# Performance work log

Hardware: AMD Instinct MI355X
Metric: run time of the kernel (lower is better)

## Reference

```python
import jax, jax.numpy as jnp
import numpy as np

# Static problem dims (match setup_inputs / torch max()+1 derivation)
N = 2_000_000      # atoms
NALT = 8           # alternatives
B, C, R = 8, 4, 512  # batch, chains, residues
N_ATOM_TYPES = 500
VDW_COL = 0        # property_hashings['solvenergy_props']['VdW']
PADDING_INDEX = -1
BACKBONE_ATOMS = (0, 1, 2, 3)


def setup_inputs() -> dict:
    key = jax.random.key(0)
    k1, k2, k3, k4, k5, k6, k7, k8 = jax.random.split(key, 8)
    at_name = jax.random.randint(k1, (N,), 0, 40)      # atom type hashes (first 4 = backbone)
    batch = jax.random.randint(k2, (N,), 0, B)
    chain = jax.random.randint(k3, (N,), 0, C)
    resnum = jax.random.randint(k4, (N,), 0, R)
    atom_description = jnp.stack([at_name, batch, chain, resnum], axis=1).astype(jnp.int64)
    return {
        "coords": jax.random.normal(k5, (N, 3), dtype=jnp.float32),
        "atom_description": atom_description,
        "alternativeMask": jax.random.randint(k6, (N, NALT), 0, 2).astype(bool),
        "facc": jax.random.uniform(k7, (N, NALT), dtype=jnp.float32),
        "atom_Properties": jax.random.uniform(k8, (N_ATOM_TYPES, 8), dtype=jnp.float32),
        "weight": jnp.zeros((1,), dtype=jnp.float32),
    }


def reference(coords, atom_description, alternativeMask, facc, atom_Properties, weight):
    at_name = atom_description[:, 0]
    b_idx = atom_description[:, 1]
    c_idx = atom_description[:, 2]
    r_idx = atom_description[:, 3]

    # is_backbone: OR over backbone atom hashes
    bb = jnp.asarray(BACKBONE_ATOMS)
    is_backbone = (at_name[:, None] == bb[None, :]).any(axis=-1)  # [N]

    # bindToAtoms: gather VdW property, masked multiply by max(facc, 0)
    sa = jnp.maximum(facc, jnp.float32(0.0))                 # [N, NALT]
    vdw = atom_Properties[at_name, VDW_COL]                  # [N]
    atomE = jnp.where(alternativeMask, vdw[:, None] * sa, jnp.float32(0.0))
    atomE = atomE * (1.0 - jnp.tanh(weight[0])) * 0.3        # [N, NALT]

    # bindToResi: masked scatter-add into [B, C, R, NALT]
    valid = r_idx != PADDING_INDEX
    mc_vals = jnp.where((is_backbone & valid)[:, None], atomE, jnp.float32(0.0))
    sc_vals = jnp.where((~is_backbone & valid)[:, None], atomE, jnp.float32(0.0))
    zeros = jnp.zeros((B, C, R, NALT), dtype=jnp.float32)
    finalMC = zeros.at[b_idx, c_idx, r_idx].add(mc_vals)
    finalSC = zeros.at[b_idx, c_idx, r_idx].add(sc_vals)
    return finalMC, finalSC
```

## Files before the change

kernel.cpp:

```cpp
#include <hip/hip_runtime.h>
#include <hip/hip_bf16.h>
#include <math.h>

#define NALT      8
#define BDIM      8
#define CDIM      4
#define RDIM      512
#define OUT_HALF  (BDIM * CDIM * RDIM * NALT)
#define OUT_TOTAL (2 * OUT_HALF)

#define NBUCKET   32
#define BLK_ATOMS 512
#define AITER     2
#define NWAVE     4
#define LSLOTS    8192


__device__ __forceinline__ unsigned int pack_bf16_2(float a, float b) {
    unsigned int ua = __float_as_uint(a);
    unsigned int ub = __float_as_uint(b);
    ua = (ua + 0x7fffu + ((ua >> 16) & 1u)) >> 16;
    ub = (ub + 0x7fffu + ((ub >> 16) & 1u)) >> 16;
    return ua | (ub << 16);
}

__global__ void __launch_bounds__(256) vdw_fused_kernel(
    const int4*   __restrict__ desc,
    const int4*   __restrict__ mask,
    const float4* __restrict__ facc,
    const float*  __restrict__ props,
    const float*  __restrict__ weight,
    unsigned short* __restrict__ hdrArr,
    unsigned short* __restrict__ lidxArr,
    uint4*        __restrict__ valArr,
    int n)
{
    __shared__ unsigned int   cw[NWAVE][NBUCKET];
    __shared__ unsigned int   base[NBUCKET + 1];
    __shared__ unsigned short s_lidx[BLK_ATOMS];
    __shared__ uint4          s_val[BLK_ATOMS];

    const int tid  = threadIdx.x;
    const int w    = tid >> 6;
    const int lane = tid & 63;
    if (lane < NBUCKET) cw[w][lane] = 0;

    const int a0 = blockIdx.x * BLK_ATOMS;
    int4   d_[AITER];
    float4 f0_[AITER], f1_[AITER];
    int4   m0_[AITER], m1_[AITER];
    bool   ok[AITER];
    #pragma unroll
    for (int it = 0; it < AITER; ++it) {
        const int a  = a0 + it * 256 + tid;
        ok[it] = (a < n);
        const int aa = ok[it] ? a : (n - 1);
        d_[it]  = desc[aa];
        f0_[it] = facc[aa * 2 + 0];
        f1_[it] = facc[aa * 2 + 1];
        m0_[it] = mask[aa * 2 + 0];
        m1_[it] = mask[aa * 2 + 1];
    }
    const float scale = (1.0f - tanhf(weight[0])) * 0.3f;

    int bkt[AITER];
    int lidx[AITER];
    #pragma unroll
    for (int it = 0; it < AITER; ++it) {
        const int4 d = d_[it];
        bkt[it] = -1;
        if (ok[it] && d.w != -1) {
            bkt[it]  = d.y * CDIM + d.z;
            lidx[it] = ((d.x < 4) ? 0 : 4096) + d.w * 8;
            atomicAdd(&cw[w][bkt[it]], 1u);
        }
    }

    uint4 rv[AITER];
    #pragma unroll
    for (int it = 0; it < AITER; ++it) {
        if (bkt[it] < 0) continue;
        const float vs = props[d_[it].x * 8] * scale;
        const float4 f0 = f0_[it], f1 = f1_[it];
        const int4   m0 = m0_[it], m1 = m1_[it];
        const float v0 = m0.x ? vs * fmaxf(f0.x, 0.0f) : 0.0f;
        const float v1 = m0.y ? vs * fmaxf(f0.y, 0.0f) : 0.0f;
        const float v2 = m0.z ? vs * fmaxf(f0.z, 0.0f) : 0.0f;
        const float v3 = m0.w ? vs * fmaxf(f0.w, 0.0f) : 0.0f;
        const float v4 = m1.x ? vs * fmaxf(f1.x, 0.0f) : 0.0f;
        const float v5 = m1.y ? vs * fmaxf(f1.y, 0.0f) : 0.0f;
        const float v6 = m1.z ? vs * fmaxf(f1.z, 0.0f) : 0.0f;
        const float v7 = m1.w ? vs * fmaxf(f1.w, 0.0f) : 0.0f;
        rv[it] = make_uint4(pack_bf16_2(v0, v1), pack_bf16_2(v2, v3),
                            pack_bf16_2(v4, v5), pack_bf16_2(v6, v7));
    }
    __syncthreads();

    if (tid < NBUCKET) {
        unsigned int s = 0;
        #pragma unroll
        for (int ww = 0; ww < NWAVE; ++ww) {
            const unsigned int c = cw[ww][tid];
            cw[ww][tid] = s;
            s += c;
        }
        unsigned int incl = s;
        #pragma unroll
        for (int off = 1; off < NBUCKET; off <<= 1) {
            const unsigned int t = __shfl_up(incl, off, NBUCKET);
            if (tid >= off) incl += t;
        }
        base[tid] = incl - s;
        if (tid == NBUCKET - 1) base[NBUCKET] = incl;
    }
    __syncthreads();

    #pragma unroll
    for (int it = 0; it < AITER; ++it) {
        if (bkt[it] < 0) continue;
        const unsigned int pos = base[bkt[it]] + atomicAdd(&cw[w][bkt[it]], 1u);
        s_lidx[pos] = (unsigned short)lidx[it];
        s_val[pos]  = rv[it];
    }
    __syncthreads();

    if (tid <= NBUCKET)
        hdrArr[blockIdx.x * 64 + tid] = (unsigned short)base[tid];

    unsigned int* ldst = (unsigned int*)(lidxArr + (size_t)blockIdx.x * BLK_ATOMS);
    const unsigned int* lsrc = (const unsigned int*)s_lidx;
    #pragma unroll
    for (int k = 0; k < BLK_ATOMS / 2 / 256; ++k)
        ldst[k * 256 + tid] = lsrc[k * 256 + tid];

    uint4* vdst = valArr + (size_t)blockIdx.x * BLK_ATOMS;
    #pragma unroll
    for (int k = 0; k < BLK_ATOMS / 256; ++k)
        vdst[k * 256 + tid] = s_val[k * 256 + tid];
}

__global__ void __launch_bounds__(256) vdw_accum_kernel(
    const unsigned short* __restrict__ hdrArr,
    const unsigned short* __restrict__ lidxArr,
    const uint4*          __restrict__ valArr,
    float*                __restrict__ partial,
    int nblocks, int nsplit)
{
    __shared__ float acc[LSLOTS];
    const int tid = threadIdx.x;
    for (int k = tid; k < LSLOTS; k += 256) acc[k] = 0.0f;
    __syncthreads();

    const int bucket = blockIdx.x / nsplit;
    const int split  = blockIdx.x % nsplit;
    const int per = (nblocks + nsplit - 1) / nsplit;
    const int b0  = split * per;
    const int b1  = (b0 + per < nblocks) ? (b0 + per) : nblocks;

    const int g    = tid >> 5;
    const int lane = tid & 31;

    for (int blk = b0 + g; blk < b1; blk += 8) {
        const int start = hdrArr[blk * 64 + bucket];
        const int end   = hdrArr[blk * 64 + bucket + 1];
        const unsigned short* la = lidxArr + (size_t)blk * BLK_ATOMS;
        const uint4*          va = valArr  + (size_t)blk * BLK_ATOMS;
        for (int rec = start + lane; rec < end; rec += 32) {
            const int   l = la[rec];
            const uint4 v = va[rec];
            float t;
            t = __uint_as_float(v.x << 16);          if (t != 0.0f) atomicAdd(&acc[l + 0], t);
            t = __uint_as_float(v.x & 0xffff0000u);  if (t != 0.0f) atomicAdd(&acc[l + 1], t);
            t = __uint_as_float(v.y << 16);          if (t != 0.0f) atomicAdd(&acc[l + 2], t);
            t = __uint_as_float(v.y & 0xffff0000u);  if (t != 0.0f) atomicAdd(&acc[l + 3], t);
            t = __uint_as_float(v.z << 16);          if (t != 0.0f) atomicAdd(&acc[l + 4], t);
            t = __uint_as_float(v.z & 0xffff0000u);  if (t != 0.0f) atomicAdd(&acc[l + 5], t);
            t = __uint_as_float(v.w << 16);          if (t != 0.0f) atomicAdd(&acc[l + 6], t);
            t = __uint_as_float(v.w & 0xffff0000u);  if (t != 0.0f) atomicAdd(&acc[l + 7], t);
        }
    }
    __syncthreads();

    float* dst = partial + (size_t)blockIdx.x * LSLOTS;
    for (int k = tid; k < LSLOTS; k += 256) dst[k] = acc[k];
}

__global__ void __launch_bounds__(256) vdw_merge_kernel(
    const float* __restrict__ partial,
    float*       __restrict__ out,
    int nsplit)
{
    const int idx = blockIdx.x * 256 + threadIdx.x;
    if (idx >= OUT_TOTAL) return;
    const int bb     = idx >> 17;
    const int b      = (idx >> 14) & 7;
    const int c      = (idx >> 12) & 3;
    const int lidx   = bb * 4096 + (idx & 4095);
    const int bucket = b * CDIM + c;
    const float* p = partial + ((size_t)bucket * nsplit) * LSLOTS + lidx;
    float s = 0.0f;
    for (int sp = 0; sp < nsplit; ++sp)
        s += p[(size_t)sp * LSLOTS];
    out[idx] = s;
}

__global__ void __launch_bounds__(256) vdw_atomic_kernel(
    const int*   __restrict__ desc,
    const int*   __restrict__ mask,
    const float* __restrict__ facc,
    const float* __restrict__ props,
    const float* __restrict__ weight,
    float*       __restrict__ out,
    int n)
{
    const int i = blockIdx.x * blockDim.x + threadIdx.x;
    if (i >= n) return;
    const float scale = (1.0f - tanhf(weight[0])) * 0.3f;
    const int4 d = reinterpret_cast<const int4*>(desc)[i];
    if (d.w == -1) return;
    const float vs = props[d.x * 8 + 0] * scale;
    const int   bb = (d.x >= 0 && d.x <= 3) ? 0 : 1;
    float* base = out + bb * OUT_HALF + (((d.y * CDIM + d.z) * RDIM + d.w) * NALT);
    const float4 f0 = reinterpret_cast<const float4*>(facc)[i * 2 + 0];
    const float4 f1 = reinterpret_cast<const float4*>(facc)[i * 2 + 1];
    const int4   m0 = reinterpret_cast<const int4*>(mask)[i * 2 + 0];
    const int4   m1 = reinterpret_cast<const int4*>(mask)[i * 2 + 1];
    if (m0.x) atomicAdd(base + 0, vs * fmaxf(f0.x, 0.0f));
    if (m0.y) atomicAdd(base + 1, vs * fmaxf(f0.y, 0.0f));
    if (m0.z) atomicAdd(base + 2, vs * fmaxf(f0.z, 0.0f));
    if (m0.w) atomicAdd(base + 3, vs * fmaxf(f0.w, 0.0f));
    if (m1.x) atomicAdd(base + 4, vs * fmaxf(f1.x, 0.0f));
    if (m1.y) atomicAdd(base + 5, vs * fmaxf(f1.y, 0.0f));
    if (m1.z) atomicAdd(base + 6, vs * fmaxf(f1.z, 0.0f));
    if (m1.w) atomicAdd(base + 7, vs * fmaxf(f1.w, 0.0f));
}

extern "C" void kernel_launch(void* const* d_in, const int* in_sizes, int n_in,
                              void* d_out, int out_size, void* d_ws, size_t ws_size,
                              hipStream_t stream)
{
    const int*   desc   = (const int*)d_in[1];
    const int*   mask   = (const int*)d_in[2];
    const float* facc   = (const float*)d_in[3];
    const float* props  = (const float*)d_in[4];
    const float* weight = (const float*)d_in[5];
    float*       out    = (float*)d_out;

    const int n       = in_sizes[1] / 4;
    const int nblocks = (n + BLK_ATOMS - 1) / BLK_ATOMS;

    auto align256 = [](size_t x) { return (x + 255) & ~(size_t)255; };
    const size_t off_hdr  = 0;
    const size_t off_lidx = align256(off_hdr  + (size_t)nblocks * 64 * 2);
    const size_t off_val  = align256(off_lidx + (size_t)nblocks * BLK_ATOMS * 2);
    const size_t off_part = align256(off_val  + (size_t)nblocks * BLK_ATOMS * 16);

    int nsplit = 0;
    for (int cand = 16; cand >= 1; cand >>= 1) {
        const size_t need = off_part +
            (size_t)NBUCKET * cand * LSLOTS * sizeof(float);
        if (need <= ws_size) { nsplit = cand; break; }
    }

    if (nsplit >= 1) {
        char* ws = (char*)d_ws;
        unsigned short* hdrArr  = (unsigned short*)(ws + off_hdr);
        unsigned short* lidxArr = (unsigned short*)(ws + off_lidx);
        uint4*          valArr  = (uint4*)(ws + off_val);
        float*          part    = (float*)(ws + off_part);

        vdw_fused_kernel<<<nblocks, 256, 0, stream>>>(
            (const int4*)desc, (const int4*)mask, (const float4*)facc,
            props, weight, hdrArr, lidxArr, valArr, n);

        vdw_accum_kernel<<<NBUCKET * nsplit, 256, 0, stream>>>(
            hdrArr, lidxArr, valArr, part, nblocks, nsplit);

        vdw_merge_kernel<<<(OUT_TOTAL + 255) / 256, 256, 0, stream>>>(
            part, out, nsplit);
    } else {
        hipMemsetAsync(d_out, 0, (size_t)out_size * sizeof(float), stream);
        vdw_atomic_kernel<<<(n + 255) / 256, 256, 0, stream>>>(
            desc, mask, facc, props, weight, out, n);
    }
}
```

Baseline: 87.53 us.

## Stage facc/mask loads via direct global-to-LDS DMA and vectorize merge

The fused binning kernel now issues global_load_lds DMA transfers for the facc and mask rows into shared memory instead of loading them into registers. The bucket prefix scan now runs before the values are consumed, so the loads can overlap the histogram and scan work and register pressure drops. The merge kernel now sums four output slots per thread using float4 loads and stores. This adds 32KB of LDS per block, which may reduce occupancy, and it depends on the DMA completing before the post-barrier reads.

```diff
diff --git a/kernel.cpp b/kernel.cpp
--- a/kernel.cpp
+++ b/kernel.cpp
@@ -15,6 +15,10 @@
 #define NWAVE     4
 #define LSLOTS    8192
 
+
+#define DMA16(gp, lp) __builtin_amdgcn_global_load_lds(                        \
+    (const __attribute__((address_space(1))) unsigned int*)(gp),               \
+    (__attribute__((address_space(3))) unsigned int*)(lp), 16, 0, 0)
 
 __device__ __forceinline__ unsigned int pack_bf16_2(float a, float b) {
     unsigned int ua = __float_as_uint(a);
@@ -35,6 +39,7 @@
     uint4*        __restrict__ valArr,
     int n)
 {
+    __shared__ __align__(16) char s_fm[NWAVE * AITER * 4 * 64 * 16];
     __shared__ unsigned int   cw[NWAVE][NBUCKET];
     __shared__ unsigned int   base[NBUCKET + 1];
     __shared__ unsigned short s_lidx[BLK_ATOMS];
@@ -46,20 +51,22 @@
     if (lane < NBUCKET) cw[w][lane] = 0;
 
     const int a0 = blockIdx.x * BLK_ATOMS;
-    int4   d_[AITER];
-    float4 f0_[AITER], f1_[AITER];
-    int4   m0_[AITER], m1_[AITER];
-    bool   ok[AITER];
+
+    int4 d_[AITER];
+    bool ok[AITER];
     #pragma unroll
     for (int it = 0; it < AITER; ++it) {
         const int a  = a0 + it * 256 + tid;
         ok[it] = (a < n);
         const int aa = ok[it] ? a : (n - 1);
-        d_[it]  = desc[aa];
-        f0_[it] = facc[aa * 2 + 0];
-        f1_[it] = facc[aa * 2 + 1];
-        m0_[it] = mask[aa * 2 + 0];
-        m1_[it] = mask[aa * 2 + 1];
+        const int c8 = w * AITER + it;
+        const float4* gf = facc + (size_t)aa * 2;
+        const int4*   gm = mask + (size_t)aa * 2;
+        DMA16(gf,     &s_fm[(c8 * 4 + 0) * 1024]);
+        DMA16(gf + 1, &s_fm[(c8 * 4 + 1) * 1024]);
+        DMA16(gm,     &s_fm[(c8 * 4 + 2) * 1024]);
+        DMA16(gm + 1, &s_fm[(c8 * 4 + 3) * 1024]);
+        d_[it] = desc[aa];
     }
     const float scale = (1.0f - tanhf(weight[0])) * 0.3f;
 
@@ -75,14 +82,36 @@
             atomicAdd(&cw[w][bkt[it]], 1u);
         }
     }
-
-    uint4 rv[AITER];
+    __syncthreads();
+
+    if (tid < NBUCKET) {
+        unsigned int s = 0;
+        #pragma unroll
+        for (int ww = 0; ww < NWAVE; ++ww) {
+            const unsigned int c = cw[ww][tid];
+            cw[ww][tid] = s;
+            s += c;
+        }
+        unsigned int incl = s;
+        #pragma unroll
+        for (int off = 1; off < NBUCKET; off <<= 1) {
+            const unsigned int t = __shfl_up(incl, off, NBUCKET);
+            if (tid >= off) incl += t;
+        }
+        base[tid] = incl - s;
+        if (tid == NBUCKET - 1) base[NBUCKET] = incl;
+    }
+    __syncthreads();
+
     #pragma unroll
     for (int it = 0; it < AITER; ++it) {
         if (bkt[it] < 0) continue;
+        const int c8 = w * AITER + it;
+        const float4 f0 = *(const float4*)&s_fm[(c8 * 4 + 0) * 1024 + lane * 16];
+        const float4 f1 = *(const float4*)&s_fm[(c8 * 4 + 1) * 1024 + lane * 16];
+        const int4   m0 = *(const int4*)  &s_fm[(c8 * 4 + 2) * 1024 + lane * 16];
+        const int4   m1 = *(const int4*)  &s_fm[(c8 * 4 + 3) * 1024 + lane * 16];
         const float vs = props[d_[it].x * 8] * scale;
-        const float4 f0 = f0_[it], f1 = f1_[it];
-        const int4   m0 = m0_[it], m1 = m1_[it];
         const float v0 = m0.x ? vs * fmaxf(f0.x, 0.0f) : 0.0f;
         const float v1 = m0.y ? vs * fmaxf(f0.y, 0.0f) : 0.0f;
         const float v2 = m0.z ? vs * fmaxf(f0.z, 0.0f) : 0.0f;
@@ -91,36 +120,11 @@
         const float v5 = m1.y ? vs * fmaxf(f1.y, 0.0f) : 0.0f;
         const float v6 = m1.z ? vs * fmaxf(f1.z, 0.0f) : 0.0f;
         const float v7 = m1.w ? vs * fmaxf(f1.w, 0.0f) : 0.0f;
-        rv[it] = make_uint4(pack_bf16_2(v0, v1), pack_bf16_2(v2, v3),
-                            pack_bf16_2(v4, v5), pack_bf16_2(v6, v7));
-    }
-    __syncthreads();
-
-    if (tid < NBUCKET) {
-        unsigned int s = 0;
-        #pragma unroll
-        for (int ww = 0; ww < NWAVE; ++ww) {
-            const unsigned int c = cw[ww][tid];
-            cw[ww][tid] = s;
-            s += c;
-        }
-        unsigned int incl = s;
-        #pragma unroll
-        for (int off = 1; off < NBUCKET; off <<= 1) {
-            const unsigned int t = __shfl_up(incl, off, NBUCKET);
-            if (tid >= off) incl += t;
-        }
-        base[tid] = incl - s;
-        if (tid == NBUCKET - 1) base[NBUCKET] = incl;
-    }
-    __syncthreads();
-
-    #pragma unroll
-    for (int it = 0; it < AITER; ++it) {
-        if (bkt[it] < 0) continue;
+        const uint4 rv = make_uint4(pack_bf16_2(v0, v1), pack_bf16_2(v2, v3),
+                                    pack_bf16_2(v4, v5), pack_bf16_2(v6, v7));
         const unsigned int pos = base[bkt[it]] + atomicAdd(&cw[w][bkt[it]], 1u);
         s_lidx[pos] = (unsigned short)lidx[it];
-        s_val[pos]  = rv[it];
+        s_val[pos]  = rv;
     }
     __syncthreads();
 
@@ -190,18 +194,21 @@
     float*       __restrict__ out,
     int nsplit)
 {
-    const int idx = blockIdx.x * 256 + threadIdx.x;
-    if (idx >= OUT_TOTAL) return;
+    const int q = blockIdx.x * 256 + threadIdx.x;
+    if (q * 4 >= OUT_TOTAL) return;
+    const int idx = q * 4;
     const int bb     = idx >> 17;
     const int b      = (idx >> 14) & 7;
     const int c      = (idx >> 12) & 3;
     const int lidx   = bb * 4096 + (idx & 4095);
     const int bucket = b * CDIM + c;
     const float* p = partial + ((size_t)bucket * nsplit) * LSLOTS + lidx;
-    float s = 0.0f;
-    for (int sp = 0; sp < nsplit; ++sp)
-        s += p[(size_t)sp * LSLOTS];
-    out[idx] = s;
+    float4 s = make_float4(0.f, 0.f, 0.f, 0.f);
+    for (int sp = 0; sp < nsplit; ++sp) {
+        const float4 v = *(const float4*)(p + (size_t)sp * LSLOTS);
+        s.x += v.x; s.y += v.y; s.z += v.z; s.w += v.w;
+    }
+    *(float4*)&out[idx] = s;
 }
 
 __global__ void __launch_bounds__(256) vdw_atomic_kernel(
@@ -276,7 +283,7 @@
         vdw_accum_kernel<<<NBUCKET * nsplit, 256, 0, stream>>>(
             hdrArr, lidxArr, valArr, part, nblocks, nsplit);
 
-        vdw_merge_kernel<<<(OUT_TOTAL + 255) / 256, 256, 0, stream>>>(
+        vdw_merge_kernel<<<(OUT_TOTAL / 4 + 255) / 256, 256, 0, stream>>>(
             part, out, nsplit);
     } else {
         hipMemsetAsync(d_out, 0, (size_t)out_size * sizeof(float), stream);
```

New measurement: 87.38 us. About the same (-0.2%).
